# Optimization experiments

Hardware: AMD Instinct MI355X
Metric: run time of the kernel (lower is better)

The kernel has to match this reference:

```python
import jax, jax.numpy as jnp
import numpy as np

B, D, H, W = 1, 768, 224, 224

def _gelu(x):
    # torch nn.GELU() default = exact erf gelu
    return jax.nn.gelu(x, approximate=False)

def _forward(query_semantic, positive_proto, negative_proto, boundary_proto, spatial_map,
             alpha_w1, alpha_b1, alpha_w2, alpha_b2,
             neg_w1, neg_b1, neg_w2, neg_b2,
             prompt_w, prompt_b, dec_w, dec_b, logit_w, logit_b):
    Bb, _, Hs, Ws = spatial_map.shape
    fused = jnp.concatenate([positive_proto, negative_proto, boundary_proto], axis=-1)  # (B, 3D)
    alpha = jax.nn.sigmoid(_gelu(fused @ alpha_w1 + alpha_b1) @ alpha_w2 + alpha_b2)  # (B, 1)
    neg_lambda = jax.nn.sigmoid(_gelu(negative_proto @ neg_w1 + neg_b1) @ neg_w2 + neg_b2)  # (B, 1)
    prompt_tokens = (fused @ prompt_w + prompt_b)[:, None, :]  # (B, 1, D)
    # 1x1 conv over spatially-constant broadcast maps == per-batch matmul, then broadcast.
    dec_vec = fused @ dec_w + dec_b  # (B, D)
    decoder_feature_bias_map = jnp.broadcast_to(dec_vec[:, :, None, None], (Bb, dec_vec.shape[1], Hs, Ws))
    semantic_prototype_map = alpha[:, :, None, None] * jnp.broadcast_to(
        positive_proto[:, :, None, None], spatial_map.shape)
    diff = boundary_proto - negative_proto  # channel-norm is spatially invariant
    sb = jnp.sqrt(jnp.sum(diff * diff, axis=-1, keepdims=True))  # (B, 1)
    spatial_bias_map = jnp.broadcast_to(sb[:, :, None, None], (Bb, 1, Hs, Ws))
    logit_dec = dec_vec @ logit_w + logit_b          # (B, 1)
    logit_neg = negative_proto @ logit_w + logit_b   # (B, 1)
    ml = logit_dec - neg_lambda * logit_neg
    mask_logit_bias_map = jnp.broadcast_to(ml[:, :, None, None], (Bb, 1, Hs, Ws))
    semantic_prototype = alpha * positive_proto + (1.0 - alpha) * query_semantic  # (B, D)
    return (prompt_tokens, semantic_prototype, semantic_prototype_map, spatial_bias_map,
            decoder_feature_bias_map, mask_logit_bias_map, alpha, neg_lambda)

def setup_inputs() -> dict:
    key = jax.random.key(0)
    ks = jax.random.split(key, 20)
    s = 0.02
    inp = {
        'query_semantic': jax.random.normal(ks[0], (B, D), jnp.float32),
        'positive_proto': jax.random.normal(ks[1], (B, D), jnp.float32),
        'negative_proto': jax.random.normal(ks[2], (B, D), jnp.float32),
        'boundary_proto': jax.random.normal(ks[3], (B, D), jnp.float32),
        'spatial_map': jax.random.normal(ks[4], (B, D, H, W), jnp.float32),
        'alpha_w1': jax.random.normal(ks[5], (3 * D, D), jnp.float32) * s,
        'alpha_b1': jax.random.normal(ks[6], (D,), jnp.float32) * s,
        'alpha_w2': jax.random.normal(ks[7], (D, 1), jnp.float32) * s,
        'alpha_b2': jax.random.normal(ks[8], (1,), jnp.float32) * s,
        'neg_w1': jax.random.normal(ks[9], (D, D), jnp.float32) * s,
        'neg_b1': jax.random.normal(ks[10], (D,), jnp.float32) * s,
        'neg_w2': jax.random.normal(ks[11], (D, 1), jnp.float32) * s,
        'neg_b2': jax.random.normal(ks[12], (1,), jnp.float32) * s,
        'prompt_w': jax.random.normal(ks[13], (3 * D, D), jnp.float32) * s,
        'prompt_b': jax.random.normal(ks[14], (D,), jnp.float32) * s,
        'dec_w': jax.random.normal(ks[15], (3 * D, D), jnp.float32) * s,
        'dec_b': jax.random.normal(ks[16], (D,), jnp.float32) * s,
        'logit_w': jax.random.normal(ks[17], (D, 1), jnp.float32) * s,
        'logit_b': jax.random.normal(ks[18], (1,), jnp.float32) * s,
    }
    return inp

def reference(query_semantic, positive_proto, negative_proto, boundary_proto, spatial_map,
              alpha_w1, alpha_b1, alpha_w2, alpha_b2,
              neg_w1, neg_b1, neg_w2, neg_b2,
              prompt_w, prompt_b, dec_w, dec_b, logit_w, logit_b):
    return _forward(query_semantic, positive_proto, negative_proto, boundary_proto, spatial_map,
                    alpha_w1, alpha_b1, alpha_w2, alpha_b2,
                    neg_w1, neg_b1, neg_w2, neg_b2,
                    prompt_w, prompt_b, dec_w, dec_b, logit_w, logit_b)
```

## Files before the change

### kernel.cpp

```cpp
#include <hip/hip_runtime.h>
#include <math.h>

#define DD     768
#define NPIX   50176
#define NPIX4  12544
#define NK     16

typedef float f4 __attribute__((ext_vector_type(4)));

#define WS_PART 0
#define WS_TBL  (4*NK*DD)

#define O_PROMPT 0
#define O_SP     (O_PROMPT + DD)
#define O_SPM    (O_SP + DD)
#define O_SB     (O_SPM + (size_t)DD*NPIX)
#define O_DEC    (O_SB + NPIX)
#define O_ML     (O_DEC + (size_t)DD*NPIX)
#define O_ALPHA  (O_ML + NPIX)
#define O_NL     (O_ALPHA + 1)

__device__ __forceinline__ float gelu_exact(float x) {
    return 0.5f * x * (1.0f + erff(x * 0.70710678118654752f));
}
__device__ __forceinline__ float sigmoidf(float x) {
    return 1.0f / (1.0f + expf(-x));
}

__global__ __launch_bounds__(256) void k_matvec_part(
    const float* __restrict__ pos, const float* __restrict__ neg,
    const float* __restrict__ bnd,
    const float* __restrict__ alpha_w1, const float* __restrict__ prompt_w,
    const float* __restrict__ dec_w,   const float* __restrict__ neg_w1,
    float* __restrict__ ws)
{
    const int kchunk = blockIdx.x, jchunk = blockIdx.y, m = blockIdx.z;
    const int tid = threadIdx.x;
    const int j = jchunk * 256 + tid;

    const float* W = (m == 0) ? alpha_w1 : (m == 1) ? prompt_w
                   : (m == 2) ? dec_w    : neg_w1;

    __shared__ float xs[144];
    if (m == 3) {
        const int k0 = kchunk * 48;
        if (tid < 48) xs[tid] = neg[k0 + tid];
    } else {
        const int k0 = kchunk * 144;
        if (tid < 144) {
            int k = k0 + tid;
            float v;
            if (k < DD)          v = pos[k];
            else if (k < 2 * DD) v = neg[k - DD];
            else                 v = bnd[k - 2 * DD];
            xs[tid] = v;
        }
    }
    __syncthreads();

    float acc = 0.0f;
    if (m == 3) {
        const float* Wp = W + (size_t)(kchunk * 48) * DD + j;
        #pragma unroll 24
        for (int kk = 0; kk < 48; ++kk)
            acc += xs[kk] * Wp[(size_t)kk * DD];
    } else {
        const float* Wp = W + (size_t)(kchunk * 144) * DD + j;
        #pragma unroll 24
        for (int kk = 0; kk < 144; ++kk)
            acc += xs[kk] * Wp[(size_t)kk * DD];
    }

    ws[WS_PART + (size_t)(m * NK + kchunk) * DD + j] = acc;
}

__global__ __launch_bounds__(768) void k_small(
    const float* __restrict__ query, const float* __restrict__ pos,
    const float* __restrict__ neg,   const float* __restrict__ bnd,
    const float* __restrict__ alpha_b1, const float* __restrict__ alpha_w2,
    const float* __restrict__ alpha_b2,
    const float* __restrict__ neg_b1,   const float* __restrict__ neg_w2,
    const float* __restrict__ neg_b2,
    const float* __restrict__ prompt_b, const float* __restrict__ dec_b,
    const float* __restrict__ logit_w,  const float* __restrict__ logit_b,
    float* __restrict__ ws, float* __restrict__ out)
{
    const int j = threadIdx.x;

    float a_h = 0.f, pr = 0.f, dc = 0.f, ng = 0.f;
    #pragma unroll
    for (int c = 0; c < NK; ++c) {
        a_h += ws[WS_PART + (0 * NK + c) * DD + j];
        pr  += ws[WS_PART + (1 * NK + c) * DD + j];
        dc  += ws[WS_PART + (2 * NK + c) * DD + j];
        ng  += ws[WS_PART + (3 * NK + c) * DD + j];
    }

    pr += prompt_b[j];
    const float dec_v = dc + dec_b[j];
    out[O_PROMPT + j]       = pr;
    ws[WS_TBL + 769 + j]    = dec_v;

    const float ga   = gelu_exact(a_h + alpha_b1[j]);
    const float gn   = gelu_exact(ng  + neg_b1[j]);
    const float negj = neg[j];
    const float lw   = logit_w[j];
    const float dbd  = bnd[j] - negj;

    float r[5];
    r[0] = ga * alpha_w2[j];
    r[1] = gn * neg_w2[j];
    r[2] = dec_v * lw;
    r[3] = negj * lw;
    r[4] = dbd * dbd;

    #pragma unroll
    for (int s = 32; s > 0; s >>= 1) {
        #pragma unroll
        for (int q = 0; q < 5; ++q) r[q] += __shfl_xor(r[q], s, 64);
    }

    __shared__ float red[5][12];
    const int wid = j >> 6, lane = j & 63;
    if (lane == 0) {
        #pragma unroll
        for (int q = 0; q < 5; ++q) red[q][wid] = r[q];
    }
    __syncthreads();

    __shared__ float sh_alpha;
    if (j == 0) {
        float s[5];
        #pragma unroll
        for (int q = 0; q < 5; ++q) {
            float t = 0.f;
            #pragma unroll
            for (int w = 0; w < 12; ++w) t += red[q][w];
            s[q] = t;
        }
        const float alpha = sigmoidf(s[0] + alpha_b2[0]);
        const float nl    = sigmoidf(s[1] + neg_b2[0]);
        const float ld    = s[2] + logit_b[0];
        const float ln    = s[3] + logit_b[0];
        out[O_ALPHA]       = alpha;
        out[O_NL]          = nl;
        ws[WS_TBL + 768]   = sqrtf(s[4]);
        ws[WS_TBL + 1537]  = ld - nl * ln;
        sh_alpha = alpha;
    }
    __syncthreads();

    const float alpha = sh_alpha;
    const float ap    = alpha * pos[j];
    out[O_SP + j]  = ap + (1.0f - alpha) * query[j];
    ws[WS_TBL + j] = ap;
}

__global__ __launch_bounds__(256) void k_fill(
    const float* __restrict__ ws, float* __restrict__ out)
{
    const float* tbl = ws + WS_TBL;
    f4* p = (f4*)(out + O_SPM);
    const unsigned total  = 1538u * NPIX4;
    const unsigned stride = gridDim.x * 256u;
    for (unsigned i = blockIdx.x * 256u + threadIdx.x; i < total; i += stride) {
        const unsigned c = i / NPIX4;
        const float v = tbl[c];
        f4 v4 = {v, v, v, v};
        __builtin_nontemporal_store(v4, p + i);
    }
}

extern "C" void kernel_launch(void* const* d_in, const int* in_sizes, int n_in,
                              void* d_out, int out_size, void* d_ws, size_t ws_size,
                              hipStream_t stream) {
    const float* query    = (const float*)d_in[0];
    const float* pos      = (const float*)d_in[1];
    const float* neg      = (const float*)d_in[2];
    const float* bnd      = (const float*)d_in[3];
    const float* alpha_w1 = (const float*)d_in[5];
    const float* alpha_b1 = (const float*)d_in[6];
    const float* alpha_w2 = (const float*)d_in[7];
    const float* alpha_b2 = (const float*)d_in[8];
    const float* neg_w1   = (const float*)d_in[9];
    const float* neg_b1   = (const float*)d_in[10];
    const float* neg_w2   = (const float*)d_in[11];
    const float* neg_b2   = (const float*)d_in[12];
    const float* prompt_w = (const float*)d_in[13];
    const float* prompt_b = (const float*)d_in[14];
    const float* dec_w    = (const float*)d_in[15];
    const float* dec_b    = (const float*)d_in[16];
    const float* logit_w  = (const float*)d_in[17];
    const float* logit_b  = (const float*)d_in[18];

    float* out = (float*)d_out;
    float* ws  = (float*)d_ws;

    k_matvec_part<<<dim3(NK, 3, 4), 256, 0, stream>>>(
        pos, neg, bnd, alpha_w1, prompt_w, dec_w, neg_w1, ws);

    k_small<<<1, DD, 0, stream>>>(
        query, pos, neg, bnd,
        alpha_b1, alpha_w2, alpha_b2,
        neg_b1, neg_w2, neg_b2,
        prompt_b, dec_b, logit_w, logit_b,
        ws, out);

    k_fill<<<2048, 256, 0, stream>>>(ws, out);
}
```

Before: 68.56 us.

## Fuse matvec, glue and broadcast fill into one persistent kernel with atomic sync

Merges the three launches into one kernel of 1536 blocks. The first 160 blocks compute vectorized partial matvecs and signal a counter, one glue block waits on it, does the reductions and scalars, then sets a flag. All blocks spin on that flag before writing the broadcast fill. This removes launch gaps and spreads the matvec over more blocks with f4 loads. In exchange it relies on the worker blocks being resident at the same time, needs an extra memset launch, and leaves every fill block waiting on the glue.

```diff
diff --git a/kernel.cpp b/kernel.cpp
--- a/kernel.cpp
+++ b/kernel.cpp
@@ -4,12 +4,15 @@
 #define DD     768
 #define NPIX   50176
 #define NPIX4  12544
-#define NK     16
+#define NBLK   1536
+#define NMVB   160
+#define GLUEB  160
 
 typedef float f4 __attribute__((ext_vector_type(4)));
 
 #define WS_PART 0
-#define WS_TBL  (4*NK*DD)
+#define WS_TBL  (NMVB*DD)
+#define WS_SYNC (WS_TBL + 1544)
 
 #define O_PROMPT 0
 #define O_SP     (O_PROMPT + DD)
@@ -27,143 +30,157 @@
     return 1.0f / (1.0f + expf(-x));
 }
 
-__global__ __launch_bounds__(256) void k_matvec_part(
-    const float* __restrict__ pos, const float* __restrict__ neg,
-    const float* __restrict__ bnd,
-    const float* __restrict__ alpha_w1, const float* __restrict__ prompt_w,
-    const float* __restrict__ dec_w,   const float* __restrict__ neg_w1,
-    float* __restrict__ ws)
-{
-    const int kchunk = blockIdx.x, jchunk = blockIdx.y, m = blockIdx.z;
-    const int tid = threadIdx.x;
-    const int j = jchunk * 256 + tid;
-
-    const float* W = (m == 0) ? alpha_w1 : (m == 1) ? prompt_w
-                   : (m == 2) ? dec_w    : neg_w1;
-
-    __shared__ float xs[144];
-    if (m == 3) {
-        const int k0 = kchunk * 48;
-        if (tid < 48) xs[tid] = neg[k0 + tid];
-    } else {
-        const int k0 = kchunk * 144;
-        if (tid < 144) {
-            int k = k0 + tid;
-            float v;
-            if (k < DD)          v = pos[k];
-            else if (k < 2 * DD) v = neg[k - DD];
-            else                 v = bnd[k - 2 * DD];
-            xs[tid] = v;
-        }
-    }
-    __syncthreads();
-
-    float acc = 0.0f;
-    if (m == 3) {
-        const float* Wp = W + (size_t)(kchunk * 48) * DD + j;
-        #pragma unroll 24
-        for (int kk = 0; kk < 48; ++kk)
-            acc += xs[kk] * Wp[(size_t)kk * DD];
-    } else {
-        const float* Wp = W + (size_t)(kchunk * 144) * DD + j;
-        #pragma unroll 24
-        for (int kk = 0; kk < 144; ++kk)
-            acc += xs[kk] * Wp[(size_t)kk * DD];
-    }
-
-    ws[WS_PART + (size_t)(m * NK + kchunk) * DD + j] = acc;
-}
-
-__global__ __launch_bounds__(768) void k_small(
+__global__ __launch_bounds__(256, 6) void k_fused(
     const float* __restrict__ query, const float* __restrict__ pos,
     const float* __restrict__ neg,   const float* __restrict__ bnd,
-    const float* __restrict__ alpha_b1, const float* __restrict__ alpha_w2,
-    const float* __restrict__ alpha_b2,
-    const float* __restrict__ neg_b1,   const float* __restrict__ neg_w2,
-    const float* __restrict__ neg_b2,
-    const float* __restrict__ prompt_b, const float* __restrict__ dec_b,
+    const float* __restrict__ alpha_w1, const float* __restrict__ alpha_b1,
+    const float* __restrict__ alpha_w2, const float* __restrict__ alpha_b2,
+    const float* __restrict__ neg_w1,   const float* __restrict__ neg_b1,
+    const float* __restrict__ neg_w2,   const float* __restrict__ neg_b2,
+    const float* __restrict__ prompt_w, const float* __restrict__ prompt_b,
+    const float* __restrict__ dec_w,    const float* __restrict__ dec_b,
     const float* __restrict__ logit_w,  const float* __restrict__ logit_b,
     float* __restrict__ ws, float* __restrict__ out)
 {
-    const int j = threadIdx.x;
-
-    float a_h = 0.f, pr = 0.f, dc = 0.f, ng = 0.f;
-    #pragma unroll
-    for (int c = 0; c < NK; ++c) {
-        a_h += ws[WS_PART + (0 * NK + c) * DD + j];
-        pr  += ws[WS_PART + (1 * NK + c) * DD + j];
-        dc  += ws[WS_PART + (2 * NK + c) * DD + j];
-        ng  += ws[WS_PART + (3 * NK + c) * DD + j];
+    const int b = blockIdx.x;
+    const int t = threadIdx.x;
+    unsigned* ctr  = (unsigned*)(ws + WS_SYNC);
+    unsigned* flag = ctr + 1;
+
+    if (b < NMVB) {
+        int m, c;
+        if (b < 144) { m = b / 48; c = b % 48; }
+        else         { m = 3;      c = b - 144; }
+        const float* W = (m == 0) ? alpha_w1 : (m == 1) ? prompt_w
+                       : (m == 2) ? dec_w    : neg_w1;
+        const int k0 = c * 48;
+
+        __shared__ float xs[48];
+        if (t < 48) {
+            int k = k0 + t;
+            float v;
+            if (m == 3)           v = neg[k];
+            else if (k < DD)      v = pos[k];
+            else if (k < 2 * DD)  v = neg[k - DD];
+            else                  v = bnd[k - 2 * DD];
+            xs[t] = v;
+        }
+        __syncthreads();
+
+        if (t < 192) {
+            const int j0 = 4 * t;
+            f4 acc = {0.f, 0.f, 0.f, 0.f};
+            const float* Wp = W + (size_t)k0 * DD + j0;
+            #pragma unroll 8
+            for (int kk = 0; kk < 48; ++kk)
+                acc += xs[kk] * (*(const f4*)(Wp + (size_t)kk * DD));
+            *(f4*)(ws + WS_PART + (size_t)b * DD + j0) = acc;
+        }
+        __syncthreads();
+        if (t == 0) { __threadfence(); atomicAdd(ctr, 1u); }
+    } else if (b == GLUEB) {
+        if (t == 0) {
+            while (atomicAdd(ctr, 0u) < (unsigned)NMVB) __builtin_amdgcn_s_sleep(8);
+            __threadfence();
+        }
+        __syncthreads();
+
+        float r0 = 0.f, r1 = 0.f, r2 = 0.f, r3 = 0.f, r4 = 0.f;
+        if (t < 192) {
+            const int j0 = 4 * t;
+            const float* P = ws + WS_PART;
+            f4 ah = {0,0,0,0}, pr = {0,0,0,0}, dc = {0,0,0,0}, ng = {0,0,0,0};
+            #pragma unroll 8
+            for (int c = 0; c < 48; ++c) ah += *(const f4*)(P + (size_t)c * DD + j0);
+            #pragma unroll 8
+            for (int c = 0; c < 48; ++c) pr += *(const f4*)(P + (size_t)(48 + c) * DD + j0);
+            #pragma unroll 8
+            for (int c = 0; c < 48; ++c) dc += *(const f4*)(P + (size_t)(96 + c) * DD + j0);
+            #pragma unroll 8
+            for (int c = 0; c < 16; ++c) ng += *(const f4*)(P + (size_t)(144 + c) * DD + j0);
+
+            pr += *(const f4*)(prompt_b + j0);
+            const f4 dec_v = dc + *(const f4*)(dec_b + j0);
+            *(f4*)(out + O_PROMPT + j0) = pr;
+            #pragma unroll
+            for (int u = 0; u < 4; ++u)
+                ws[WS_TBL + 769 + j0 + u] = dec_v[u];
+
+            const f4 ab1  = *(const f4*)(alpha_b1 + j0);
+            const f4 nb1  = *(const f4*)(neg_b1   + j0);
+            const f4 aw2  = *(const f4*)(alpha_w2 + j0);
+            const f4 nw2  = *(const f4*)(neg_w2   + j0);
+            const f4 lw   = *(const f4*)(logit_w  + j0);
+            const f4 negj = *(const f4*)(neg      + j0);
+            const f4 bndj = *(const f4*)(bnd      + j0);
+            #pragma unroll
+            for (int u = 0; u < 4; ++u) {
+                const float ga  = gelu_exact(ah[u] + ab1[u]);
+                const float gn  = gelu_exact(ng[u] + nb1[u]);
+                const float dbd = bndj[u] - negj[u];
+                r0 += ga * aw2[u];
+                r1 += gn * nw2[u];
+                r2 += dec_v[u] * lw[u];
+                r3 += negj[u] * lw[u];
+                r4 += dbd * dbd;
+            }
+        }
+
+        #pragma unroll
+        for (int s = 32; s > 0; s >>= 1) {
+            r0 += __shfl_xor(r0, s, 64);
+            r1 += __shfl_xor(r1, s, 64);
+            r2 += __shfl_xor(r2, s, 64);
+            r3 += __shfl_xor(r3, s, 64);
+            r4 += __shfl_xor(r4, s, 64);
+        }
+        __shared__ float red[5][4];
+        __shared__ float sh_alpha;
+        const int wid = t >> 6;
+        if ((t & 63) == 0) {
+            red[0][wid] = r0; red[1][wid] = r1; red[2][wid] = r2;
+            red[3][wid] = r3; red[4][wid] = r4;
+        }
+        __syncthreads();
+        if (t == 0) {
+            float s0 = red[0][0] + red[0][1] + red[0][2] + red[0][3];
+            float s1 = red[1][0] + red[1][1] + red[1][2] + red[1][3];
+            float s2 = red[2][0] + red[2][1] + red[2][2] + red[2][3];
+            float s3 = red[3][0] + red[3][1] + red[3][2] + red[3][3];
+            float s4 = red[4][0] + red[4][1] + red[4][2] + red[4][3];
+            const float alpha = sigmoidf(s0 + alpha_b2[0]);
+            const float nl    = sigmoidf(s1 + neg_b2[0]);
+            const float ld    = s2 + logit_b[0];
+            const float ln    = s3 + logit_b[0];
+            out[O_ALPHA]      = alpha;
+            out[O_NL]         = nl;
+            ws[WS_TBL + 768]  = sqrtf(s4);
+            ws[WS_TBL + 1537] = ld - nl * ln;
+            sh_alpha = alpha;
+        }
+        __syncthreads();
+        if (t < 192) {
+            const int j0 = 4 * t;
+            const float alpha = sh_alpha;
+            const f4 ap = alpha * (*(const f4*)(pos + j0));
+            *(f4*)(out + O_SP + j0) = ap + (1.0f - alpha) * (*(const f4*)(query + j0));
+            *(f4*)(ws + WS_TBL + j0) = ap;
+        }
+        __syncthreads();
+        if (t == 0) { __threadfence(); atomicExch(flag, 1u); }
     }
 
-    pr += prompt_b[j];
-    const float dec_v = dc + dec_b[j];
-    out[O_PROMPT + j]       = pr;
-    ws[WS_TBL + 769 + j]    = dec_v;
-
-    const float ga   = gelu_exact(a_h + alpha_b1[j]);
-    const float gn   = gelu_exact(ng  + neg_b1[j]);
-    const float negj = neg[j];
-    const float lw   = logit_w[j];
-    const float dbd  = bnd[j] - negj;
-
-    float r[5];
-    r[0] = ga * alpha_w2[j];
-    r[1] = gn * neg_w2[j];
-    r[2] = dec_v * lw;
-    r[3] = negj * lw;
-    r[4] = dbd * dbd;
-
-    #pragma unroll
-    for (int s = 32; s > 0; s >>= 1) {
-        #pragma unroll
-        for (int q = 0; q < 5; ++q) r[q] += __shfl_xor(r[q], s, 64);
-    }
-
-    __shared__ float red[5][12];
-    const int wid = j >> 6, lane = j & 63;
-    if (lane == 0) {
-        #pragma unroll
-        for (int q = 0; q < 5; ++q) red[q][wid] = r[q];
+    if (t == 0) {
+        while (atomicAdd(flag, 0u) == 0u) __builtin_amdgcn_s_sleep(8);
+        __threadfence();
     }
     __syncthreads();
 
-    __shared__ float sh_alpha;
-    if (j == 0) {
-        float s[5];
-        #pragma unroll
-        for (int q = 0; q < 5; ++q) {
-            float t = 0.f;
-            #pragma unroll
-            for (int w = 0; w < 12; ++w) t += red[q][w];
-            s[q] = t;
-        }
-        const float alpha = sigmoidf(s[0] + alpha_b2[0]);
-        const float nl    = sigmoidf(s[1] + neg_b2[0]);
-        const float ld    = s[2] + logit_b[0];
-        const float ln    = s[3] + logit_b[0];
-        out[O_ALPHA]       = alpha;
-        out[O_NL]          = nl;
-        ws[WS_TBL + 768]   = sqrtf(s[4]);
-        ws[WS_TBL + 1537]  = ld - nl * ln;
-        sh_alpha = alpha;
-    }
-    __syncthreads();
-
-    const float alpha = sh_alpha;
-    const float ap    = alpha * pos[j];
-    out[O_SP + j]  = ap + (1.0f - alpha) * query[j];
-    ws[WS_TBL + j] = ap;
-}
-
-__global__ __launch_bounds__(256) void k_fill(
-    const float* __restrict__ ws, float* __restrict__ out)
-{
     const float* tbl = ws + WS_TBL;
     f4* p = (f4*)(out + O_SPM);
     const unsigned total  = 1538u * NPIX4;
-    const unsigned stride = gridDim.x * 256u;
-    for (unsigned i = blockIdx.x * 256u + threadIdx.x; i < total; i += stride) {
+    const unsigned stride = NBLK * 256u;
+    for (unsigned i = (unsigned)b * 256u + (unsigned)t; i < total; i += stride) {
         const unsigned c = i / NPIX4;
         const float v = tbl[c];
         f4 v4 = {v, v, v, v};
@@ -196,15 +213,13 @@
     float* out = (float*)d_out;
     float* ws  = (float*)d_ws;
 
-    k_matvec_part<<<dim3(NK, 3, 4), 256, 0, stream>>>(
-        pos, neg, bnd, alpha_w1, prompt_w, dec_w, neg_w1, ws);
-
-    k_small<<<1, DD, 0, stream>>>(
+    hipMemsetAsync((char*)d_ws + (size_t)WS_SYNC * sizeof(float), 0,
+                   2 * sizeof(unsigned), stream);
+
+    k_fused<<<NBLK, 256, 0, stream>>>(
         query, pos, neg, bnd,
-        alpha_b1, alpha_w2, alpha_b2,
-        neg_b1, neg_w2, neg_b2,
-        prompt_b, dec_b, logit_w, logit_b,
-        ws, out);
-
-    k_fill<<<2048, 256, 0, stream>>>(ws, out);
-}
+        alpha_w1, alpha_b1, alpha_w2, alpha_b2,
+        neg_w1, neg_b1, neg_w2, neg_b2,
+        prompt_w, prompt_b, dec_w, dec_b,
+        logit_w, logit_b, ws, out);
+}
```

Result: slower. 120.1 us (+75.2%).
